# Kernel optimization log

Measured on AMD Instinct MI355X. Metric: run time of the kernel, lower is better.

The kernel has to match this reference:

```python
import jax, jax.numpy as jnp
import numpy as np

T, D, N, K = 8192, 512, 4, 5

def setup_inputs() -> dict:
    key = jax.random.key(0)
    k1, k2, k3 = jax.random.split(key, 3)
    X = jax.random.normal(k1, (T, D), dtype=jnp.float32)
    gaps = jax.random.uniform(k2, (T, N), dtype=jnp.float32)
    # random choice among the K-1 non-self nearest neighbors (randint(0, k-2) in torch)
    nn_choice = jax.random.randint(k3, (T, N), 0, K - 1)
    return {"X": X, "gaps": gaps, "nn_choice": nn_choice, "k": K}


def reference(X, gaps, nn_choice, k):
    """SMOTE.generate: pairwise euclidean dists -> kNN -> interpolate.

    X: [T, D] minority samples; gaps: [T, N] uniform(0,1);
    nn_choice: [T, N] ints in [0, k-1) selecting which neighbor.
    Returns synthetic samples [T*N, D].
    """
    # pairwise euclidean distance via the |x|^2 expansion (O(T^2 D) GEMM)
    sq = jnp.sum(X * X, axis=1)                       # [T]
    d2 = sq[:, None] + sq[None, :] - 2.0 * (X @ X.T)  # [T, T]
    dist = jnp.sqrt(jnp.maximum(d2, 0.0))
    # k smallest distances per row; column 0 is self (distance 0)
    _, idx = jax.lax.top_k(-dist, k)                  # [T, k]
    neigh = idx[:, 1:]                                # [T, k-1], drop self
    sel = jnp.take_along_axis(neigh, nn_choice, axis=1)  # [T, N]
    base = X[:, None, :]                              # [T, 1, D]
    diff = X[sel] - base                              # [T, N, D]
    synth = base + gaps[:, :, None] * diff            # [T, N, D]
    return synth.reshape(-1, X.shape[1])              # [T*N, D]
```

## Files before the change

### kernel.cpp

```cpp
#include <hip/hip_runtime.h>

#define TT 8192
#define DD 512
#define NN 4
#define JS 16
#define JR (TT / JS)
#define BIGU 0xFFFFFFFFu

typedef unsigned int uint;
typedef unsigned short ushort;
typedef __attribute__((ext_vector_type(8))) short short8;
typedef __attribute__((ext_vector_type(4))) float f32x4;

__device__ __forceinline__ uint bfr(float f) {
  uint u = __float_as_uint(f);
  return (u + 0x7FFFu + ((u >> 16) & 1u)) >> 16;
}

__global__ void cvtsq_kernel(const float* __restrict__ X, uint4* __restrict__ Xb,
                             float* __restrict__ sq) {
  int w = threadIdx.x >> 6, l = threadIdx.x & 63;
  int row = blockIdx.x * 4 + w;
  const float4* xr = (const float4*)(X + (size_t)row * DD) + l * 2;
  float4 a = xr[0], b = xr[1];
  uint4 o;
  o.x = bfr(a.x) | (bfr(a.y) << 16);
  o.y = bfr(a.z) | (bfr(a.w) << 16);
  o.z = bfr(b.x) | (bfr(b.y) << 16);
  o.w = bfr(b.z) | (bfr(b.w) << 16);
  Xb[(size_t)row * 64 + l] = o;
  float s = a.x * a.x + a.y * a.y + a.z * a.z + a.w * a.w +
            b.x * b.x + b.y * b.y + b.z * b.z + b.w * b.w;
#pragma unroll
  for (int off = 32; off >= 1; off >>= 1) s += __shfl_down(s, off, 64);
  if (l == 0) sq[row] = s;
}

__device__ __forceinline__ void gload16(const void* g, void* l) {
  __builtin_amdgcn_global_load_lds(
      (const __attribute__((address_space(1))) void*)(size_t)g,
      (__attribute__((address_space(3))) void*)(uint)(size_t)l, 16, 0, 0);
}

__device__ __forceinline__ int swz(int r) {
  return (r & 3) ^ ((r >> 1) & 2) ^ ((r >> 3) & 1);
}

__global__ __launch_bounds__(256, 4) void gemm_topk(
    const ushort* __restrict__ Xb, const float* __restrict__ sqv,
    uint* __restrict__ ckey) {
  __shared__ char smem[32768];

  const int t = threadIdx.x;
  const int w = t >> 6, l = t & 63;
  const int l15 = l & 15, q4 = l >> 4;
  const int bi = blockIdx.x >> 4;
  const int bs = blockIdx.x & 15;
  const int i0 = bi * 128;
  const int js0 = bs * JR;
  const char* XbB = (const char*)Xb;
  const int mq = (w & 1) * 64;
  const int nq = (w >> 1) * 64;

  const char* gQ[4];
#pragma unroll
  for (int q = 0; q < 4; ++q) {
    int cidx = q * 256 + t;
    int r = cidx >> 2, slot = cidx & 3;
    int cs = slot ^ swz(r);
    int rowg = (r < 128) ? (i0 + r) : (js0 + r - 128);
    gQ[q] = XbB + (size_t)rowg * 1024 + cs * 16;
  }

  uint L[4][4];
#pragma unroll
  for (int cb = 0; cb < 4; ++cb)
#pragma unroll
    for (int s = 0; s < 4; ++s) L[cb][s] = BIGU;

  f32x4 acc[4][4];
#pragma unroll
  for (int rb = 0; rb < 4; ++rb)
#pragma unroll
    for (int cb = 0; cb < 4; ++cb) {
      f32x4 z = {0.f, 0.f, 0.f, 0.f};
      acc[rb][cb] = z;
    }

  {
#pragma unroll
    for (int q = 0; q < 4; ++q)
      gload16(gQ[q], smem + (q * 256 + t) * 16);
  }

  int cellA[4], cellB[4];
#pragma unroll
  for (int rb = 0; rb < 4; ++rb) {
    int rj = 128 + mq + rb * 16 + l15;
    cellA[rb] = rj * 4 + (q4 ^ swz(rj));
  }
#pragma unroll
  for (int cb = 0; cb < 4; ++cb) {
    int ri = nq + cb * 16 + l15;
    cellB[cb] = ri * 4 + (q4 ^ swz(ri));
  }

  for (int s = 0; s < 64; ++s) {
    const int kt = s & 15, jt = s >> 4;
    __syncthreads();

    {
      const int sn = (s + 1) & 63;
      const int ioff = (sn & 15) * 64;
      const int joff = ioff + (sn >> 4) * 131072;
      char* dbase = smem + ((s + 1) & 1) * 16384;
#pragma unroll
      for (int q = 0; q < 4; ++q)
        gload16(gQ[q] + (q < 2 ? ioff : joff), dbase + (q * 256 + t) * 16);
    }

    {
      const char* base = smem + (s & 1) * 16384;
      short8 af[4], bf[4];
#pragma unroll
      for (int rb = 0; rb < 4; ++rb)
        af[rb] = *(const short8*)(base + cellA[rb] * 16);
#pragma unroll
      for (int cb = 0; cb < 4; ++cb)
        bf[cb] = *(const short8*)(base + cellB[cb] * 16);
#pragma unroll
      for (int rb = 0; rb < 4; ++rb)
#pragma unroll
        for (int cb = 0; cb < 4; ++cb)
          acc[rb][cb] = __builtin_amdgcn_mfma_f32_16x16x32_bf16(
              af[rb], bf[cb], acc[rb][cb], 0, 0, 0);
    }

    if (kt == 15) {
      const int jb = js0 + jt * 128;
#pragma unroll
      for (int rb = 0; rb < 4; ++rb) {
        int jg = jb + mq + rb * 16 + q4 * 4;
        float4 sj = *(const float4*)(sqv + jg);
        float s4[4] = {sj.x, sj.y, sj.z, sj.w};
#pragma unroll
        for (int cb = 0; cb < 4; ++cb) {
#pragma unroll
          for (int r = 0; r < 4; ++r) {
            float key = fmaf(-2.f, acc[rb][cb][r], s4[r]);
            uint u = __float_as_uint(key);
            u ^= (uint)((int)u >> 31) | 0x80000000u;
            uint p = (u & 0xFFFFE000u) | (uint)(jg + r);
            if (p < L[cb][3]) {
              L[cb][3] = p;
#pragma unroll
              for (int x = 3; x >= 1; --x) {
                uint lo = L[cb][x - 1], hi = L[cb][x];
                bool sw = hi < lo;
                L[cb][x - 1] = sw ? hi : lo;
                L[cb][x] = sw ? lo : hi;
              }
            }
          }
        }
      }
#pragma unroll
      for (int rb = 0; rb < 4; ++rb)
#pragma unroll
        for (int cb = 0; cb < 4; ++cb) {
          f32x4 z = {0.f, 0.f, 0.f, 0.f};
          acc[rb][cb] = z;
        }
    }
  }

  __syncthreads();
  uint* ml = (uint*)smem;
  const int cid = (w & 1) * 4 + q4;
#pragma unroll
  for (int cb = 0; cb < 4; ++cb) {
    int n = nq + cb * 16 + l15;
#pragma unroll
    for (int s = 0; s < 4; ++s) ml[n * 33 + cid * 4 + s] = L[cb][s];
  }
  __syncthreads();
  if (t < 128) {
    uint best[8];
#pragma unroll
    for (int s = 0; s < 8; ++s) best[s] = BIGU;
    for (int u = 0; u < 32; ++u) {
      uint p = ml[t * 33 + u];
      if (p < best[7]) {
        best[7] = p;
#pragma unroll
        for (int s = 7; s >= 1; --s) {
          uint lo = best[s - 1], hi = best[s];
          bool sw = hi < lo;
          best[s - 1] = sw ? hi : lo;
          best[s] = sw ? lo : hi;
        }
      }
    }
#pragma unroll
    for (int s = 0; s < 8; ++s)
      ckey[(size_t)(i0 + t) * 128 + bs * 8 + s] = best[s];
  }
}

__global__ __launch_bounds__(256) void refine_gen(
    const float* __restrict__ X, const uint* __restrict__ ckey,
    const float* __restrict__ gaps, const int* __restrict__ nnc,
    float* __restrict__ out) {
  __shared__ uint keys[4][128];
  __shared__ uint seln[4][8];
  const int w = threadIdx.x >> 6, l = threadIdx.x & 63;
  const int row = blockIdx.x * 4 + w;
  uint k0 = ckey[(size_t)row * 128 + l];
  uint k1 = ckey[(size_t)row * 128 + 64 + l];
  keys[w][l] = k0;
  keys[w][64 + l] = k1;
  __syncthreads();

  int r0 = 0, r1 = 0;
  const uint4* kk = (const uint4*)keys[w];
#pragma unroll
  for (int i = 0; i < 32; ++i) {
    uint4 v = kk[i];
    r0 += (v.x < k0) + (v.y < k0) + (v.z < k0) + (v.w < k0);
    r1 += (v.x < k1) + (v.y < k1) + (v.z < k1) + (v.w < k1);
  }
  if (r0 < 8) seln[w][r0] = k0 & 8191u;
  if (r1 < 8) seln[w][r1] = k1 & 8191u;
  __syncthreads();

  int selj[8];
#pragma unroll
  for (int s = 0; s < 8; ++s) selj[s] = (int)seln[w][s];

  float xi[8];
  const float4* xr = (const float4*)(X + (size_t)row * DD) + l * 2;
  float4 xa = xr[0], xb = xr[1];
  xi[0] = xa.x; xi[1] = xa.y; xi[2] = xa.z; xi[3] = xa.w;
  xi[4] = xb.x; xi[5] = xb.y; xi[6] = xb.z; xi[7] = xb.w;

  float yv[8][8];
  double ex[8];
#pragma unroll
  for (int s = 0; s < 8; ++s) {
    const float4* yr = (const float4*)(X + (size_t)selj[s] * DD) + l * 2;
    float4 ya = yr[0], yb = yr[1];
    yv[s][0] = ya.x; yv[s][1] = ya.y; yv[s][2] = ya.z; yv[s][3] = ya.w;
    yv[s][4] = yb.x; yv[s][5] = yb.y; yv[s][6] = yb.z; yv[s][7] = yb.w;
    double a = 0.0;
#pragma unroll
    for (int m = 0; m < 8; ++m) {
      double df = (double)xi[m] - (double)yv[s][m];
      a += df * df;
    }
#pragma unroll
    for (int off = 32; off >= 1; off >>= 1) a += __shfl_down(a, off, 64);
    ex[s] = __shfl(a, 0, 64);
  }

  int rk[8];
#pragma unroll
  for (int s = 0; s < 8; ++s) {
    int r = 0;
#pragma unroll
    for (int u = 0; u < 8; ++u)
      if (ex[u] < ex[s] || (ex[u] == ex[s] && selj[u] < selj[s])) ++r;
    rk[s] = r;
  }

#pragma unroll
  for (int o = 0; o < 4; ++o) {
    float g = gaps[row * 4 + o];
    int target = nnc[row * 4 + o] + 1;
    float ys[8];
#pragma unroll
    for (int m = 0; m < 8; ++m) ys[m] = 0.f;
#pragma unroll
    for (int s = 0; s < 8; ++s) {
      bool hit = (rk[s] == target);
#pragma unroll
      for (int m = 0; m < 8; ++m) ys[m] = hit ? yv[s][m] : ys[m];
    }
    float4 r0v, r1v;
    r0v.x = fmaf(g, ys[0] - xi[0], xi[0]);
    r0v.y = fmaf(g, ys[1] - xi[1], xi[1]);
    r0v.z = fmaf(g, ys[2] - xi[2], xi[2]);
    r0v.w = fmaf(g, ys[3] - xi[3], xi[3]);
    r1v.x = fmaf(g, ys[4] - xi[4], xi[4]);
    r1v.y = fmaf(g, ys[5] - xi[5], xi[5]);
    r1v.z = fmaf(g, ys[6] - xi[6], xi[6]);
    r1v.w = fmaf(g, ys[7] - xi[7], xi[7]);
    float4* dst = (float4*)(out + ((size_t)row * 4 + o) * DD) + l * 2;
    dst[0] = r0v;
    dst[1] = r1v;
  }
}

extern "C" void kernel_launch(void* const* d_in, const int* in_sizes, int n_in,
                              void* d_out, int out_size, void* d_ws, size_t ws_size,
                              hipStream_t stream) {
  const float* X = (const float*)d_in[0];
  const float* gaps = (const float*)d_in[1];
  const int* nnc = (const int*)d_in[2];
  float* out = (float*)d_out;

  float* sqv = (float*)d_ws;
  uint4* Xb4 = (uint4*)((char*)d_ws + 32768);
  uint* ckey = (uint*)((char*)d_ws + 32768 + 8388608);

  cvtsq_kernel<<<TT / 4, 256, 0, stream>>>(X, Xb4, sqv);
  gemm_topk<<<1024, 256, 0, stream>>>((const ushort*)Xb4, sqv, ckey);
  refine_gen<<<TT / 4, 256, 0, stream>>>(X, ckey, gaps, nnc, out);
}
```

Before: 210.2 us.

## Retile distance GEMM to 256x256 output tiles with deep LDS pipeline and per-tile top-4

```diff
diff --git a/kernel.cpp b/kernel.cpp
--- a/kernel.cpp
+++ b/kernel.cpp
@@ -2,9 +2,6 @@
 
 #define TT 8192
 #define DD 512
-#define NN 4
-#define JS 16
-#define JR (TT / JS)
 #define BIGU 0xFFFFFFFFu
 
 typedef unsigned int uint;
@@ -46,164 +43,168 @@
   return (r & 3) ^ ((r >> 1) & 2) ^ ((r >> 3) & 1);
 }
 
-__global__ __launch_bounds__(256, 4) void gemm_topk(
+__device__ __forceinline__ uint umin_(uint a, uint b) { return a < b ? a : b; }
+__device__ __forceinline__ uint umax_(uint a, uint b) { return a > b ? a : b; }
+
+__global__ __launch_bounds__(512, 2) void gemm_topk(
     const ushort* __restrict__ Xb, const float* __restrict__ sqv,
     uint* __restrict__ ckey) {
-  __shared__ char smem[32768];
+  __shared__ char smem[131072];
 
   const int t = threadIdx.x;
   const int w = t >> 6, l = t & 63;
   const int l15 = l & 15, q4 = l >> 4;
-  const int bi = blockIdx.x >> 4;
-  const int bs = blockIdx.x & 15;
-  const int i0 = bi * 128;
-  const int js0 = bs * JR;
+  const int wm = w >> 2, wn = w & 3;
+
+  const int bid = blockIdx.x;
+  const int sw = (bid & 7) * 128 + (bid >> 3);
+  const int g = sw >> 8, rr = sw & 255;
+  const int bi = rr >> 3, bj = g * 8 + (rr & 7);
+  const int i0 = bi * 256, j0 = bj * 256;
   const char* XbB = (const char*)Xb;
-  const int mq = (w & 1) * 64;
-  const int nq = (w >> 1) * 64;
-
-  const char* gQ[4];
-#pragma unroll
-  for (int q = 0; q < 4; ++q) {
-    int cidx = q * 256 + t;
-    int r = cidx >> 2, slot = cidx & 3;
-    int cs = slot ^ swz(r);
-    int rowg = (r < 128) ? (i0 + r) : (js0 + r - 128);
-    gQ[q] = XbB + (size_t)rowg * 1024 + cs * 16;
-  }
-
-  uint L[4][4];
-#pragma unroll
-  for (int cb = 0; cb < 4; ++cb)
-#pragma unroll
-    for (int s = 0; s < 4; ++s) L[cb][s] = BIGU;
-
-  f32x4 acc[4][4];
-#pragma unroll
-  for (int rb = 0; rb < 4; ++rb)
-#pragma unroll
-    for (int cb = 0; cb < 4; ++cb) {
+
+  const int cell0 = w * 128 + l, cell1 = w * 128 + 64 + l;
+  const int r0 = cell0 >> 2, c0 = cell0 & 3;
+  const int r1 = cell1 >> 2, c1 = cell1 & 3;
+  const char* sA0 = XbB + (size_t)(i0 + r0) * 1024 + (c0 ^ swz(r0)) * 16;
+  const char* sA1 = XbB + (size_t)(i0 + r1) * 1024 + (c1 ^ swz(r1)) * 16;
+  const char* sB0 = XbB + (size_t)(j0 + r0) * 1024 + (c0 ^ swz(r0)) * 16;
+  const char* sB1 = XbB + (size_t)(j0 + r1) * 1024 + (c1 ^ swz(r1)) * 16;
+  const int d0 = cell0 * 16, d1 = cell1 * 16;
+
+  int aOff[2][4], bOff[4];
+#pragma unroll
+  for (int mh = 0; mh < 2; ++mh)
+#pragma unroll
+    for (int mf = 0; mf < 4; ++mf) {
+      int row = wm * 128 + mh * 64 + mf * 16 + l15;
+      aOff[mh][mf] = row * 64 + (q4 ^ swz(row)) * 16;
+    }
+#pragma unroll
+  for (int nf = 0; nf < 4; ++nf) {
+    int row = wn * 64 + nf * 16 + l15;
+    bOff[nf] = row * 64 + (q4 ^ swz(row)) * 16;
+  }
+
+  f32x4 acc[8][4];
+#pragma unroll
+  for (int i = 0; i < 8; ++i)
+#pragma unroll
+    for (int j = 0; j < 4; ++j) {
       f32x4 z = {0.f, 0.f, 0.f, 0.f};
-      acc[rb][cb] = z;
-    }
-
-  {
-#pragma unroll
-    for (int q = 0; q < 4; ++q)
-      gload16(gQ[q], smem + (q * 256 + t) * 16);
-  }
-
-  int cellA[4], cellB[4];
-#pragma unroll
-  for (int rb = 0; rb < 4; ++rb) {
-    int rj = 128 + mq + rb * 16 + l15;
-    cellA[rb] = rj * 4 + (q4 ^ swz(rj));
-  }
-#pragma unroll
-  for (int cb = 0; cb < 4; ++cb) {
-    int ri = nq + cb * 16 + l15;
-    cellB[cb] = ri * 4 + (q4 ^ swz(ri));
-  }
-
-  for (int s = 0; s < 64; ++s) {
-    const int kt = s & 15, jt = s >> 4;
-    __syncthreads();
-
-    {
-      const int sn = (s + 1) & 63;
-      const int ioff = (sn & 15) * 64;
-      const int joff = ioff + (sn >> 4) * 131072;
-      char* dbase = smem + ((s + 1) & 1) * 16384;
-#pragma unroll
-      for (int q = 0; q < 4; ++q)
-        gload16(gQ[q] + (q < 2 ? ioff : joff), dbase + (q * 256 + t) * 16);
-    }
-
-    {
-      const char* base = smem + (s & 1) * 16384;
+      acc[i][j] = z;
+    }
+
+#pragma unroll
+  for (int h = 0; h < 6; ++h) {
+    const int tt = h >> 2, s = h & 3;
+    const int doff = (tt & 1) * 65536 + (s & 1) * 32768 + (s >> 1) * 16384;
+    const int kb = tt * 128 + (s >> 1) * 64;
+    gload16(((s & 1) ? sB0 : sA0) + kb, smem + doff + d0);
+    gload16(((s & 1) ? sB1 : sA1) + kb, smem + doff + d1);
+  }
+  asm volatile("s_waitcnt vmcnt(4)" ::: "memory");
+  __builtin_amdgcn_s_barrier();
+
+  for (int tk = 0; tk < 8; ++tk) {
+    const char* rbuf = smem + (tk & 1) * 65536;
+#pragma unroll
+    for (int p = 0; p < 4; ++p) {
+      const int kh = p >> 1, mh = p & 1;
+      const char* rbA = rbuf + kh * 16384;
+      const char* rbB = rbA + 32768;
       short8 af[4], bf[4];
 #pragma unroll
-      for (int rb = 0; rb < 4; ++rb)
-        af[rb] = *(const short8*)(base + cellA[rb] * 16);
-#pragma unroll
-      for (int cb = 0; cb < 4; ++cb)
-        bf[cb] = *(const short8*)(base + cellB[cb] * 16);
-#pragma unroll
-      for (int rb = 0; rb < 4; ++rb)
-#pragma unroll
-        for (int cb = 0; cb < 4; ++cb)
-          acc[rb][cb] = __builtin_amdgcn_mfma_f32_16x16x32_bf16(
-              af[rb], bf[cb], acc[rb][cb], 0, 0, 0);
-    }
-
-    if (kt == 15) {
-      const int jb = js0 + jt * 128;
-#pragma unroll
-      for (int rb = 0; rb < 4; ++rb) {
-        int jg = jb + mq + rb * 16 + q4 * 4;
-        float4 sj = *(const float4*)(sqv + jg);
-        float s4[4] = {sj.x, sj.y, sj.z, sj.w};
-#pragma unroll
-        for (int cb = 0; cb < 4; ++cb) {
-#pragma unroll
-          for (int r = 0; r < 4; ++r) {
-            float key = fmaf(-2.f, acc[rb][cb][r], s4[r]);
-            uint u = __float_as_uint(key);
-            u ^= (uint)((int)u >> 31) | 0x80000000u;
-            uint p = (u & 0xFFFFE000u) | (uint)(jg + r);
-            if (p < L[cb][3]) {
-              L[cb][3] = p;
-#pragma unroll
-              for (int x = 3; x >= 1; --x) {
-                uint lo = L[cb][x - 1], hi = L[cb][x];
-                bool sw = hi < lo;
-                L[cb][x - 1] = sw ? hi : lo;
-                L[cb][x] = sw ? lo : hi;
-              }
-            }
-          }
+      for (int mf = 0; mf < 4; ++mf)
+        af[mf] = *(const short8*)(rbA + aOff[mh][mf]);
+#pragma unroll
+      for (int nf = 0; nf < 4; ++nf)
+        bf[nf] = *(const short8*)(rbB + bOff[nf]);
+
+      {
+        const int s = (6 + p) & 3;
+        const int tt = tk + ((p < 2) ? 1 : 2);
+        const int doff = (tt & 1) * 65536 + (s & 1) * 32768 + (s >> 1) * 16384;
+        const int kb = (tt & 7) * 128 + (s >> 1) * 64;
+        gload16(((s & 1) ? sB0 : sA0) + kb, smem + doff + d0);
+        gload16(((s & 1) ? sB1 : sA1) + kb, smem + doff + d1);
+      }
+
+      __builtin_amdgcn_s_setprio(1);
+#pragma unroll
+      for (int mf = 0; mf < 4; ++mf)
+#pragma unroll
+        for (int nf = 0; nf < 4; ++nf)
+          acc[mh * 4 + mf][nf] = __builtin_amdgcn_mfma_f32_16x16x32_bf16(
+              af[mf], bf[nf], acc[mh * 4 + mf][nf], 0, 0, 0);
+      __builtin_amdgcn_s_setprio(0);
+
+      if (p == 3) asm volatile("s_waitcnt vmcnt(4)" ::: "memory");
+      __builtin_amdgcn_s_barrier();
+    }
+  }
+
+  asm volatile("s_waitcnt vmcnt(0)" ::: "memory");
+  __builtin_amdgcn_s_barrier();
+  asm volatile("" ::: "memory");
+
+  uint* cand = (uint*)smem;
+  float sqj[4];
+  uint jglo[4];
+#pragma unroll
+  for (int nf = 0; nf < 4; ++nf) {
+    int jg = j0 + wn * 64 + nf * 16 + l15;
+    jglo[nf] = (uint)jg;
+    sqj[nf] = sqv[jg];
+  }
+#pragma unroll
+  for (int mf = 0; mf < 8; ++mf)
+#pragma unroll
+    for (int rg = 0; rg < 4; ++rg) {
+      uint k[4];
+#pragma unroll
+      for (int nf = 0; nf < 4; ++nf) {
+        float key = fmaf(-2.f, acc[mf][nf][rg], sqj[nf]);
+        uint u = __float_as_uint(key);
+        u ^= (uint)((int)u >> 31) | 0x80000000u;
+        k[nf] = (u & 0xFFFFE000u) | jglo[nf];
+      }
+      uint a = umin_(k[0], k[1]), b = umax_(k[0], k[1]);
+      uint c = umin_(k[2], k[3]), d = umax_(k[2], k[3]);
+      uint f1 = umin_(a, c);
+      uint f2 = umin_(umax_(a, c), umin_(b, d));
+      int row = wm * 128 + mf * 16 + q4 * 4 + rg;
+      int col = wn * 32 + l15 * 2;
+      cand[row * 128 + ((col + row) & 127)] = f1;
+      cand[row * 128 + ((col + 1 + row) & 127)] = f2;
+    }
+
+  asm volatile("s_waitcnt lgkmcnt(0)" ::: "memory");
+  __builtin_amdgcn_s_barrier();
+  asm volatile("" ::: "memory");
+
+  if (t < 256) {
+    uint best[4] = {BIGU, BIGU, BIGU, BIGU};
+    const uint* rp = cand + t * 128;
+#pragma unroll 4
+    for (int u = 0; u < 128; ++u) {
+      uint p = rp[(u + t) & 127];
+      if (p < best[3]) {
+        best[3] = p;
+#pragma unroll
+        for (int x = 3; x >= 1; --x) {
+          uint lo = best[x - 1], hi = best[x];
+          bool swp = hi < lo;
+          best[x - 1] = swp ? hi : lo;
+          best[x] = swp ? lo : hi;
         }
       }
-#pragma unroll
-      for (int rb = 0; rb < 4; ++rb)
-#pragma unroll
-        for (int cb = 0; cb < 4; ++cb) {
-          f32x4 z = {0.f, 0.f, 0.f, 0.f};
-          acc[rb][cb] = z;
-        }
-    }
-  }
-
-  __syncthreads();
-  uint* ml = (uint*)smem;
-  const int cid = (w & 1) * 4 + q4;
-#pragma unroll
-  for (int cb = 0; cb < 4; ++cb) {
-    int n = nq + cb * 16 + l15;
-#pragma unroll
-    for (int s = 0; s < 4; ++s) ml[n * 33 + cid * 4 + s] = L[cb][s];
-  }
-  __syncthreads();
-  if (t < 128) {
-    uint best[8];
-#pragma unroll
-    for (int s = 0; s < 8; ++s) best[s] = BIGU;
-    for (int u = 0; u < 32; ++u) {
-      uint p = ml[t * 33 + u];
-      if (p < best[7]) {
-        best[7] = p;
-#pragma unroll
-        for (int s = 7; s >= 1; --s) {
-          uint lo = best[s - 1], hi = best[s];
-          bool sw = hi < lo;
-          best[s - 1] = sw ? hi : lo;
-          best[s] = sw ? lo : hi;
-        }
-      }
-    }
-#pragma unroll
-    for (int s = 0; s < 8; ++s)
-      ckey[(size_t)(i0 + t) * 128 + bs * 8 + s] = best[s];
+    }
+    uint* op = ckey + (size_t)(i0 + t) * 128 + bj * 4;
+    op[0] = best[0];
+    op[1] = best[1];
+    op[2] = best[2];
+    op[3] = best[3];
   }
 }
 
@@ -313,6 +314,6 @@
   uint* ckey = (uint*)((char*)d_ws + 32768 + 8388608);
 
   cvtsq_kernel<<<TT / 4, 256, 0, stream>>>(X, Xb4, sqv);
-  gemm_topk<<<1024, 256, 0, stream>>>((const ushort*)Xb4, sqv, ckey);
+  gemm_topk<<<1024, 512, 0, stream>>>((const ushort*)Xb4, sqv, ckey);
   refine_gen<<<TT / 4, 256, 0, stream>>>(X, ckey, gaps, nnc, out);
 }
```

New measurement: 230.4 us. 9.6% more time.
